# Performance work log

Measured on AMD Instinct MI355X. Metric: run time of the kernel, lower is better.

Reference implementation:

```python
import jax, jax.numpy as jnp
import numpy as np

B, N, NIN, NH, NOUT = 32, 64, 256, 256, 2
E = N * (N - 1)
BN_EPS = 1e-5


def _xavier(k, fan_in, fan_out):
    return jax.random.normal(k, (fan_in, fan_out), jnp.float32) * np.sqrt(2.0 / (fan_in + fan_out))


def _mlp_params(key, n_in, n_hid, n_out):
    k1, k2 = jax.random.split(key)
    return {
        'w1': _xavier(k1, n_in, n_hid), 'b1': jnp.full((n_hid,), 0.1, jnp.float32),
        'w2': _xavier(k2, n_hid, n_out), 'b2': jnp.full((n_out,), 0.1, jnp.float32),
        'g': jnp.ones((n_out,), jnp.float32), 'beta': jnp.zeros((n_out,), jnp.float32),
    }


def setup_inputs() -> dict:
    key = jax.random.key(0)
    ks = jax.random.split(key, 7)
    inputs = jax.random.normal(ks[0], (B, N, NIN), jnp.float32)
    # fully-connected directed graph w/o self loops: edge e = (send i, recv j), i != j
    idx = np.array([(i, j) for i in range(N) for j in range(N) if i != j], dtype=np.int64)
    rel_send = np.zeros((E, N), np.float32)
    rel_rec = np.zeros((E, N), np.float32)
    rel_send[np.arange(E), idx[:, 0]] = 1.0
    rel_rec[np.arange(E), idx[:, 1]] = 1.0
    out = {'inputs': inputs, 'rel_rec': jnp.asarray(rel_rec), 'rel_send': jnp.asarray(rel_send)}
    for name, (ni, nh, no), k in [('mlp1', (NIN, NH, NH), ks[1]),
                                  ('mlp2', (2 * NH, NH, NH), ks[2]),
                                  ('mlp3', (NH, NH, NH), ks[3]),
                                  ('mlp4', (3 * NH, NH, NH), ks[4])]:
        p = _mlp_params(k, ni, nh, no)
        for pk, pv in p.items():
            out[f'{name}_{pk}'] = pv
    out['fc_w'] = _xavier(ks[5], NH, NOUT)
    out['fc_b'] = jnp.full((NOUT,), 0.1, jnp.float32)
    return out


def _mlp(x, w1, b1, w2, b2, g, beta):
    # Linear -> ELU -> Linear -> ELU -> BatchNorm1d (training-mode batch stats, biased var)
    h = jax.nn.elu(x @ w1 + b1)
    h = jax.nn.elu(h @ w2 + b2)
    mean = h.mean(axis=(0, 1))
    var = h.var(axis=(0, 1))
    return (h - mean) * jax.lax.rsqrt(var + BN_EPS) * g + beta


def reference(inputs, rel_rec, rel_send,
              mlp1_w1, mlp1_b1, mlp1_w2, mlp1_b2, mlp1_g, mlp1_beta,
              mlp2_w1, mlp2_b1, mlp2_w2, mlp2_b2, mlp2_g, mlp2_beta,
              mlp3_w1, mlp3_b1, mlp3_w2, mlp3_b2, mlp3_g, mlp3_beta,
              mlp4_w1, mlp4_b1, mlp4_w2, mlp4_b2, mlp4_g, mlp4_beta,
              fc_w, fc_b):
    x = _mlp(inputs, mlp1_w1, mlp1_b1, mlp1_w2, mlp1_b2, mlp1_g, mlp1_beta)  # [B,N,NH]
    # node2edge: gather sender/receiver node features per edge
    s = jnp.einsum('en,bnh->beh', rel_send, x)
    r = jnp.einsum('en,bnh->beh', rel_rec, x)
    x = jnp.concatenate([s, r], axis=-1)  # [B,E,2*NH]
    x = _mlp(x, mlp2_w1, mlp2_b1, mlp2_w2, mlp2_b2, mlp2_g, mlp2_beta)
    x_skip = x
    # edge2node: scatter-sum incoming edges per node, normalized by N
    inc = jnp.einsum('en,beh->bnh', rel_rec, x) / N
    x = _mlp(inc, mlp3_w1, mlp3_b1, mlp3_w2, mlp3_b2, mlp3_g, mlp3_beta)
    s = jnp.einsum('en,bnh->beh', rel_send, x)
    r = jnp.einsum('en,bnh->beh', rel_rec, x)
    x = jnp.concatenate([s, r, x_skip], axis=-1)  # [B,E,3*NH]
    x = _mlp(x, mlp4_w1, mlp4_b1, mlp4_w2, mlp4_b2, mlp4_g, mlp4_beta)
    return x @ fc_w + fc_b  # [B,E,NOUT]
```

## Files before the change

kernel.cpp:

```cpp
#include <hip/hip_runtime.h>

typedef __bf16 bf16_t;
typedef __bf16 bf16x8 __attribute__((ext_vector_type(8)));
typedef float  f32x4  __attribute__((ext_vector_type(4)));

#define NB    64
#define EB    4032
#define BATCH 32
#define H     256
#define M_EDGE (BATCH*EB)
#define M_NODE (BATCH*NB)
#define T2    4
#define BN_EPS 1e-5f

__device__ __forceinline__ void load_lds16(const void* g, void* l) {
    __builtin_amdgcn_global_load_lds(
        (const __attribute__((address_space(1))) unsigned int*)g,
        (__attribute__((address_space(3))) unsigned int*)l, 16, 0, 0);
}
__device__ __forceinline__ float elu(float v) { return v > 0.f ? v : __expf(v) - 1.f; }

template<bool AF32>
__global__ __launch_bounds__(256)
void fused_mlp(const void* __restrict__ A0v,
               const bf16_t* __restrict__ W1t, const float* __restrict__ b1,
               const bf16_t* __restrict__ W2t, const float* __restrict__ b2,
               bf16_t* __restrict__ out, float* __restrict__ stats)
{
    const int m0 = blockIdx.x * 64;
    const int tid = threadIdx.x, wave = tid >> 6, lane = tid & 63;
    const int l15 = lane & 15, quad = lane >> 4;
    const int row = tid >> 2;
    const int cx8 = (((tid & 3) ^ ((tid >> 3) & 3))) * 8;
    const int sl8 = (tid & 3) * 8;
    const int xq8 = (quad ^ ((l15 >> 1) & 3)) * 8;

    __shared__ bf16_t h1s[64 * 264];
    __shared__ bf16_t Bs[256 * 32];
    __shared__ float  sred[512];

    const bf16_t* A0 = (const bf16_t*)A0v;

    f32x4 acc1[4][4];
#pragma unroll
    for (int t = 0; t < 4; ++t)
#pragma unroll
        for (int u = 0; u < 4; ++u) acc1[t][u] = (f32x4){0.f, 0.f, 0.f, 0.f};

    for (int k0 = 0; k0 < 256; k0 += 32) {
        bf16_t* ldsA = h1s + wave * 512;
        if (AF32) {
            const float* af = (const float*)A0v + (size_t)(m0 + row) * 256 + k0 + cx8;
            float4 lo = *(const float4*)af;
            float4 hi = *(const float4*)(af + 4);
            bf16x8 v;
            v[0]=(bf16_t)lo.x; v[1]=(bf16_t)lo.y; v[2]=(bf16_t)lo.z; v[3]=(bf16_t)lo.w;
            v[4]=(bf16_t)hi.x; v[5]=(bf16_t)hi.y; v[6]=(bf16_t)hi.z; v[7]=(bf16_t)hi.w;
            *(bf16x8*)&h1s[row * 32 + sl8] = v;
        } else {
            load_lds16(A0 + (size_t)(m0 + row) * 256 + k0 + cx8, ldsA);
        }
#pragma unroll
        for (int p = 0; p < 4; ++p)
            load_lds16(W1t + (size_t)(p * 64 + row) * 256 + k0 + cx8,
                       Bs + (p * 256 + wave * 64) * 8);
        __syncthreads();
        bf16x8 afr[4], bfr[4];
#pragma unroll
        for (int t = 0; t < 4; ++t)
            afr[t] = *(const bf16x8*)&h1s[(t * 16 + l15) * 32 + xq8];
#pragma unroll
        for (int u = 0; u < 4; ++u)
            bfr[u] = *(const bf16x8*)&Bs[(wave * 64 + u * 16 + l15) * 32 + xq8];
#pragma unroll
        for (int t = 0; t < 4; ++t)
#pragma unroll
            for (int u = 0; u < 4; ++u)
                acc1[t][u] = __builtin_amdgcn_mfma_f32_16x16x32_bf16(afr[t], bfr[u], acc1[t][u], 0, 0, 0);
        __syncthreads();
    }

#pragma unroll
    for (int u = 0; u < 4; ++u) {
        int   col = wave * 64 + u * 16 + l15;
        float bv  = b1[col];
#pragma unroll
        for (int t = 0; t < 4; ++t)
#pragma unroll
            for (int r = 0; r < 4; ++r)
                h1s[(t * 16 + quad * 4 + r) * 264 + col] = (bf16_t)elu(acc1[t][u][r] + bv);
    }
    sred[tid] = 0.f; sred[256 + tid] = 0.f;
    __syncthreads();

    f32x4 acc2[4][4];
#pragma unroll
    for (int t = 0; t < 4; ++t)
#pragma unroll
        for (int u = 0; u < 4; ++u) acc2[t][u] = (f32x4){0.f, 0.f, 0.f, 0.f};

    for (int k0 = 0; k0 < 256; k0 += 32) {
#pragma unroll
        for (int p = 0; p < 4; ++p)
            load_lds16(W2t + (size_t)(p * 64 + row) * 256 + k0 + cx8,
                       Bs + (p * 256 + wave * 64) * 8);
        __syncthreads();
        bf16x8 afr[4], bfr[4];
#pragma unroll
        for (int t = 0; t < 4; ++t)
            afr[t] = *(const bf16x8*)&h1s[(t * 16 + l15) * 264 + k0 + quad * 8];
#pragma unroll
        for (int u = 0; u < 4; ++u)
            bfr[u] = *(const bf16x8*)&Bs[(wave * 64 + u * 16 + l15) * 32 + xq8];
#pragma unroll
        for (int t = 0; t < 4; ++t)
#pragma unroll
            for (int u = 0; u < 4; ++u)
                acc2[t][u] = __builtin_amdgcn_mfma_f32_16x16x32_bf16(afr[t], bfr[u], acc2[t][u], 0, 0, 0);
        __syncthreads();
    }

#pragma unroll
    for (int u = 0; u < 4; ++u) {
        int   col = wave * 64 + u * 16 + l15;
        float bv  = b2[col];
        float s = 0.f, q = 0.f;
#pragma unroll
        for (int t = 0; t < 4; ++t)
#pragma unroll
            for (int r = 0; r < 4; ++r) {
                float v = elu(acc2[t][u][r] + bv);
                h1s[(t * 16 + quad * 4 + r) * 264 + col] = (bf16_t)v;
                s += v; q += v * v;
            }
        s += __shfl_xor(s, 16); s += __shfl_xor(s, 32);
        q += __shfl_xor(q, 16); q += __shfl_xor(q, 32);
        if (quad == 0) { atomicAdd(&sred[col], s); atomicAdd(&sred[256 + col], q); }
    }
    __syncthreads();
#pragma unroll
    for (int p = 0; p < 8; ++p) {
        int idx = p * 256 + tid;
        int r = idx >> 5, ch = idx & 31;
        *(uint4*)&out[(size_t)(m0 + r) * H + ch * 8] = *(const uint4*)&h1s[r * 264 + ch * 8];
    }
    atomicAdd(&stats[tid],     sred[tid]);
    atomicAdd(&stats[H + tid], sred[256 + tid]);
}

__global__ __launch_bounds__(256)
void node_gemm(const bf16_t* __restrict__ A, const float* __restrict__ statsIn,
               const float* __restrict__ g, const float* __restrict__ beta, float Mcnt,
               const bf16_t* __restrict__ Wt, const float* __restrict__ bias,
               float* __restrict__ out)
{
    const int m0 = blockIdx.x * 64;
    const int nb = blockIdx.y * 256;
    const int tid = threadIdx.x, wave = tid >> 6, lane = tid & 63;
    const int l15 = lane & 15, quad = lane >> 4;
    const int row = tid >> 2;
    const int cx8 = (((tid & 3) ^ ((tid >> 3) & 3))) * 8;
    const int sl8 = (tid & 3) * 8;
    const int xq8 = (quad ^ ((l15 >> 1) & 3)) * 8;
    __shared__ bf16_t As[64 * 32];
    __shared__ bf16_t Bs[256 * 32];
    __shared__ float  ss[512];

    {
        float mean = statsIn[tid] / Mcnt;
        float var  = statsIn[256 + tid] / Mcnt - mean * mean;
        float scl  = g[tid] * rsqrtf(var + BN_EPS);
        ss[tid]       = scl;
        ss[256 + tid] = beta[tid] - mean * scl;
    }
    __syncthreads();

    f32x4 acc[4][4];
#pragma unroll
    for (int t = 0; t < 4; ++t)
#pragma unroll
        for (int u = 0; u < 4; ++u) acc[t][u] = (f32x4){0.f, 0.f, 0.f, 0.f};

    for (int k0 = 0; k0 < 256; k0 += 32) {
        {
            int kc = k0 + cx8;
            bf16x8 v = *(const bf16x8*)(A + (size_t)(m0 + row) * 256 + kc);
            bf16x8 w;
#pragma unroll
            for (int j = 0; j < 8; ++j)
                w[j] = (bf16_t)((float)v[j] * ss[kc + j] + ss[256 + kc + j]);
            *(bf16x8*)&As[row * 32 + sl8] = w;
        }
#pragma unroll
        for (int p = 0; p < 4; ++p)
            load_lds16(Wt + (size_t)(nb + p * 64 + row) * 256 + k0 + cx8,
                       Bs + (p * 256 + wave * 64) * 8);
        __syncthreads();
        bf16x8 afr[4], bfr[4];
#pragma unroll
        for (int t = 0; t < 4; ++t)
            afr[t] = *(const bf16x8*)&As[(t * 16 + l15) * 32 + xq8];
#pragma unroll
        for (int u = 0; u < 4; ++u)
            bfr[u] = *(const bf16x8*)&Bs[(wave * 64 + u * 16 + l15) * 32 + xq8];
#pragma unroll
        for (int t = 0; t < 4; ++t)
#pragma unroll
            for (int u = 0; u < 4; ++u)
                acc[t][u] = __builtin_amdgcn_mfma_f32_16x16x32_bf16(afr[t], bfr[u], acc[t][u], 0, 0, 0);
        __syncthreads();
    }
#pragma unroll
    for (int u = 0; u < 4; ++u) {
        int col = nb + wave * 64 + u * 16 + l15;
        float bv = bias[col];
#pragma unroll
        for (int t = 0; t < 4; ++t)
#pragma unroll
            for (int r = 0; r < 4; ++r)
                out[(size_t)(m0 + t * 16 + quad * 4 + r) * 512 + col] = acc[t][u][r] + bv;
    }
}

__global__ __launch_bounds__(256, 2)
void m2_kernel(const float* __restrict__ PQ, const bf16_t* __restrict__ W2t,
               const float* __restrict__ b2, bf16_t* __restrict__ out,
               float* __restrict__ stats)
{
    const int tile0 = blockIdx.x * T2;
    const int tid = threadIdx.x, wave = tid >> 6, lane = tid & 63;
    const int l15 = lane & 15, quad = lane >> 4;

    __shared__ bf16_t Abuf[2][64 * 264];
    __shared__ float  sred[512];

    bf16x8 Breg[32];
#pragma unroll
    for (int ks = 0; ks < 8; ++ks)
#pragma unroll
        for (int u = 0; u < 4; ++u) {
            int col = wave * 64 + u * 16 + l15;
            Breg[ks * 4 + u] = *(const bf16x8*)(W2t + (size_t)col * 256 + ks * 32 + quad * 8);
        }
    sred[tid] = 0.f; sred[256 + tid] = 0.f;

    auto computeA = [&](int t, int b) {
        int row = tid >> 2;
        int m = (tile0 + t) * 64 + row;
        int bb = m / EB, e = m - bb * EB;
        int sn = e / (NB - 1), rr = e - sn * (NB - 1);
        int rc = rr + (rr >= sn ? 1 : 0);
        const float* Prow = PQ + (size_t)(bb * NB + sn) * 512;
        const float* Qrow = PQ + (size_t)(bb * NB + rc) * 512 + 256;
        int c0 = (tid & 3) * 64;
#pragma unroll
        for (int j = 0; j < 8; ++j) {
            int c = c0 + j * 8;
            float4 p0 = *(const float4*)(Prow + c);
            float4 p1 = *(const float4*)(Prow + c + 4);
            float4 q0 = *(const float4*)(Qrow + c);
            float4 q1 = *(const float4*)(Qrow + c + 4);
            bf16x8 v;
            v[0]=(bf16_t)elu(p0.x+q0.x); v[1]=(bf16_t)elu(p0.y+q0.y);
            v[2]=(bf16_t)elu(p0.z+q0.z); v[3]=(bf16_t)elu(p0.w+q0.w);
            v[4]=(bf16_t)elu(p1.x+q1.x); v[5]=(bf16_t)elu(p1.y+q1.y);
            v[6]=(bf16_t)elu(p1.z+q1.z); v[7]=(bf16_t)elu(p1.w+q1.w);
            *(bf16x8*)&Abuf[b][row * 264 + c] = v;
        }
    };

    computeA(0, 0);
    __syncthreads();

    for (int t = 0; t < T2; ++t) {
        const int cur = t & 1, nxt = cur ^ 1;
        if (t + 1 < T2) computeA(t + 1, nxt);

        f32x4 acc[4][4];
#pragma unroll
        for (int a = 0; a < 4; ++a)
#pragma unroll
            for (int u = 0; u < 4; ++u) acc[a][u] = (f32x4){0.f, 0.f, 0.f, 0.f};
#pragma unroll
        for (int ks = 0; ks < 8; ++ks) {
            bf16x8 afr[4];
#pragma unroll
            for (int a = 0; a < 4; ++a)
                afr[a] = *(const bf16x8*)&Abuf[cur][(a * 16 + l15) * 264 + ks * 32 + quad * 8];
#pragma unroll
            for (int a = 0; a < 4; ++a)
#pragma unroll
                for (int u = 0; u < 4; ++u)
                    acc[a][u] = __builtin_amdgcn_mfma_f32_16x16x32_bf16(afr[a], Breg[ks * 4 + u], acc[a][u], 0, 0, 0);
        }
        __syncthreads();

#pragma unroll
        for (int u = 0; u < 4; ++u) {
            int   col = wave * 64 + u * 16 + l15;
            float bv  = b2[col];
            float s = 0.f, q = 0.f;
#pragma unroll
            for (int a = 0; a < 4; ++a)
#pragma unroll
                for (int r = 0; r < 4; ++r) {
                    float v = elu(acc[a][u][r] + bv);
                    Abuf[cur][(a * 16 + quad * 4 + r) * 264 + col] = (bf16_t)v;
                    s += v; q += v * v;
                }
            s += __shfl_xor(s, 16); s += __shfl_xor(s, 32);
            q += __shfl_xor(q, 16); q += __shfl_xor(q, 32);
            if (quad == 0) { atomicAdd(&sred[col], s); atomicAdd(&sred[256 + col], q); }
        }
        __syncthreads();

        size_t m0 = (size_t)(tile0 + t) * 64;
#pragma unroll
        for (int p = 0; p < 8; ++p) {
            int idx = p * 256 + tid;
            int r = idx >> 5, ch = idx & 31;
            *(uint4*)&out[(m0 + r) * H + ch * 8] = *(const uint4*)&Abuf[cur][r * 264 + ch * 8];
        }
        __syncthreads();
    }
    atomicAdd(&stats[tid],     sred[tid]);
    atomicAdd(&stats[H + tid], sred[256 + tid]);
}

__global__ __launch_bounds__(256, 2)
void m4_kernel(const bf16_t* __restrict__ h2, const bf16_t* __restrict__ Wskt,
               const float* __restrict__ RS, const bf16_t* __restrict__ W2t,
               const float* __restrict__ b2, bf16_t* __restrict__ out,
               float* __restrict__ stats)
{
    const int m0 = blockIdx.x * 64;
    const int tid = threadIdx.x, wave = tid >> 6, lane = tid & 63;
    const int l15 = lane & 15, quad = lane >> 4;
    const int row = tid >> 2;
    const int c0 = (tid & 3) * 64;

    __shared__ bf16_t h1s[64 * 264];
    __shared__ float  sred[512];

    bf16x8 Breg[32];
#pragma unroll
    for (int ks = 0; ks < 8; ++ks)
#pragma unroll
        for (int u = 0; u < 4; ++u) {
            int col = wave * 64 + u * 16 + l15;
            Breg[ks * 4 + u] = *(const bf16x8*)(Wskt + (size_t)col * 256 + ks * 32 + quad * 8);
        }
    sred[tid] = 0.f; sred[256 + tid] = 0.f;

    {
        const bf16_t* src = h2 + (size_t)(m0 + row) * 256;
#pragma unroll
        for (int j = 0; j < 8; ++j) {
            int c = c0 + j * 8;
            *(bf16x8*)&h1s[row * 264 + c] = *(const bf16x8*)(src + c);
        }
    }
    __syncthreads();

    f32x4 acc[4][4];
#pragma unroll
    for (int a = 0; a < 4; ++a)
#pragma unroll
        for (int u = 0; u < 4; ++u) acc[a][u] = (f32x4){0.f, 0.f, 0.f, 0.f};

#pragma unroll
    for (int ks = 0; ks < 8; ++ks) {
        bf16x8 afr[4];
#pragma unroll
        for (int a = 0; a < 4; ++a)
            afr[a] = *(const bf16x8*)&h1s[(a * 16 + l15) * 264 + ks * 32 + quad * 8];
#pragma unroll
        for (int a = 0; a < 4; ++a)
#pragma unroll
            for (int u = 0; u < 4; ++u)
                acc[a][u] = __builtin_amdgcn_mfma_f32_16x16x32_bf16(afr[a], Breg[ks * 4 + u], acc[a][u], 0, 0, 0);
    }

#pragma unroll
    for (int ks = 0; ks < 8; ++ks)
#pragma unroll
        for (int u = 0; u < 4; ++u) {
            int col = wave * 64 + u * 16 + l15;
            Breg[ks * 4 + u] = *(const bf16x8*)(W2t + (size_t)col * 256 + ks * 32 + quad * 8);
        }
    __syncthreads();

#pragma unroll
    for (int u = 0; u < 4; ++u) {
        int col = wave * 64 + u * 16 + l15;
#pragma unroll
        for (int a = 0; a < 4; ++a)
#pragma unroll
            for (int r = 0; r < 4; ++r)
                h1s[(a * 16 + quad * 4 + r) * 264 + col] = (bf16_t)acc[a][u][r];
    }
    __syncthreads();

    {
        int m = m0 + row;
        int bb = m / EB, e = m - bb * EB;
        int sn = e / (NB - 1), rr = e - sn * (NB - 1);
        int rc = rr + (rr >= sn ? 1 : 0);
        const float* Srow = RS + (size_t)(bb * NB + sn) * 512;
        const float* Rrow = RS + (size_t)(bb * NB + rc) * 512 + 256;
#pragma unroll
        for (int j = 0; j < 8; ++j) {
            int c = c0 + j * 8;
            bf16x8 h = *(const bf16x8*)&h1s[row * 264 + c];
            float4 s0 = *(const float4*)(Srow + c);
            float4 s1 = *(const float4*)(Srow + c + 4);
            float4 r0 = *(const float4*)(Rrow + c);
            float4 r1 = *(const float4*)(Rrow + c + 4);
            bf16x8 v;
            v[0]=(bf16_t)elu((float)h[0]+s0.x+r0.x); v[1]=(bf16_t)elu((float)h[1]+s0.y+r0.y);
            v[2]=(bf16_t)elu((float)h[2]+s0.z+r0.z); v[3]=(bf16_t)elu((float)h[3]+s0.w+r0.w);
            v[4]=(bf16_t)elu((float)h[4]+s1.x+r1.x); v[5]=(bf16_t)elu((float)h[5]+s1.y+r1.y);
            v[6]=(bf16_t)elu((float)h[6]+s1.z+r1.z); v[7]=(bf16_t)elu((float)h[7]+s1.w+r1.w);
            *(bf16x8*)&h1s[row * 264 + c] = v;
        }
    }
    __syncthreads();

#pragma unroll
    for (int a = 0; a < 4; ++a)
#pragma unroll
        for (int u = 0; u < 4; ++u) acc[a][u] = (f32x4){0.f, 0.f, 0.f, 0.f};
#pragma unroll
    for (int ks = 0; ks < 8; ++ks) {
        bf16x8 afr[4];
#pragma unroll
        for (int a = 0; a < 4; ++a)
            afr[a] = *(const bf16x8*)&h1s[(a * 16 + l15) * 264 + ks * 32 + quad * 8];
#pragma unroll
        for (int a = 0; a < 4; ++a)
#pragma unroll
            for (int u = 0; u < 4; ++u)
                acc[a][u] = __builtin_amdgcn_mfma_f32_16x16x32_bf16(afr[a], Breg[ks * 4 + u], acc[a][u], 0, 0, 0);
    }
    __syncthreads();

#pragma unroll
    for (int u = 0; u < 4; ++u) {
        int   col = wave * 64 + u * 16 + l15;
        float bv  = b2[col];
        float s = 0.f, q = 0.f;
#pragma unroll
        for (int a = 0; a < 4; ++a)
#pragma unroll
            for (int r = 0; r < 4; ++r) {
                float v = elu(acc[a][u][r] + bv);
                h1s[(a * 16 + quad * 4 + r) * 264 + col] = (bf16_t)v;
                s += v; q += v * v;
            }
        s += __shfl_xor(s, 16); s += __shfl_xor(s, 32);
        q += __shfl_xor(q, 16); q += __shfl_xor(q, 32);
        if (quad == 0) { atomicAdd(&sred[col], s); atomicAdd(&sred[256 + col], q); }
    }
    __syncthreads();

#pragma unroll
    for (int p = 0; p < 8; ++p) {
        int idx = p * 256 + tid;
        int r = idx >> 5, ch = idx & 31;
        *(uint4*)&out[(size_t)(m0 + r) * H + ch * 8] = *(const uint4*)&h1s[r * 264 + ch * 8];
    }
    atomicAdd(&stats[tid],     sred[tid]);
    atomicAdd(&stats[H + tid], sred[256 + tid]);
}

__global__ void prep(const float* __restrict__ w1a, bf16_t* __restrict__ wt1a,
                     const float* __restrict__ w1b, bf16_t* __restrict__ wt1b,
                     const float* __restrict__ w2b, bf16_t* __restrict__ wt2b,
                     const float* __restrict__ w3a, bf16_t* __restrict__ wt3a,
                     const float* __restrict__ w3b, bf16_t* __restrict__ wt3b,
                     const float* __restrict__ w4b, bf16_t* __restrict__ wt4b,
                     const float* __restrict__ w2a, bf16_t* __restrict__ wtpq,
                     const float* __restrict__ w4a, bf16_t* __restrict__ wtrs,
                     const float* __restrict__ b2a, float* __restrict__ biasPQ,
                     float* __restrict__ stats)
{
    int blk = blockIdx.x, tid = threadIdx.x;
    if (blk < 1536) {
        int grp = blk >> 8, lb = blk & 255;
        const float* w; bf16_t* wt;
        switch (grp) {
            case 0: w = w1a; wt = wt1a; break;
            case 1: w = w1b; wt = wt1b; break;
            case 2: w = w2b; wt = wt2b; break;
            case 3: w = w3a; wt = wt3a; break;
            case 4: w = w3b; wt = wt3b; break;
            default: w = w4b; wt = wt4b; break;
        }
        int idx = lb * 256 + tid;
        int k = idx >> 8, n = idx & 255;
        wt[n * 256 + k] = (bf16_t)w[idx];
    } else if (blk < 2560) {
        int lb = blk - 1536;
        const float* w = (lb < 512) ? w2a : w4a;
        bf16_t* wt = (lb < 512) ? wtpq : wtrs;
        int c = lb & 511, k = tid;
        float v = (c < 256) ? w[k * 256 + c] : w[(256 + k) * 256 + (c - 256)];
        wt[c * 256 + k] = (bf16_t)v;
    } else if (blk == 2560) {
        biasPQ[tid] = b2a[tid];
        biasPQ[256 + tid] = 0.f;
    } else {
        for (int j = 0; j < 8; ++j) stats[j * 256 + tid] = 0.f;
    }
}

__global__ void prep2(const float* __restrict__ w4a, const float* __restrict__ stats2,
                      const float* __restrict__ g2, const float* __restrict__ be2,
                      const float* __restrict__ b4a, bf16_t* __restrict__ wt,
                      float* __restrict__ bias)
{
    __shared__ float sh2s[256];
    int blk = blockIdx.x, tid = threadIdx.x;
    float mean = stats2[tid] / (float)M_EDGE;
    float var  = stats2[256 + tid] / (float)M_EDGE - mean * mean;
    float scl  = g2[tid] * rsqrtf(var + BN_EPS);
    if (blk < 256) {
        wt[blk * 256 + tid] = (bf16_t)(w4a[(512 + tid) * 256 + blk] * scl);
    } else {
        sh2s[tid] = be2[tid] - mean * scl;
        __syncthreads();
        float acc = 0.f;
        for (int k = 0; k < 256; ++k)
            acc += sh2s[k] * w4a[(512 + k) * 256 + tid];
        bias[tid] = b4a[tid] + acc;
        bias[256 + tid] = 0.f;
    }
}

__global__ void edge2node(const bf16_t* __restrict__ x2, const float* __restrict__ stats2,
                          const float* __restrict__ g2, const float* __restrict__ be2,
                          bf16_t* __restrict__ inc)
{
    int bn = blockIdx.x, bb = bn >> 6, n = bn & 63;
    int g = threadIdx.x >> 5, t = threadIdx.x & 31;
    __shared__ float part[8][256];
    __shared__ float ss[512];
    {
        int c = threadIdx.x;
        float mean = stats2[c] / (float)M_EDGE;
        float var  = stats2[256 + c] / (float)M_EDGE - mean * mean;
        float scl  = g2[c] * rsqrtf(var + BN_EPS);
        ss[c]       = scl;
        ss[256 + c] = be2[c] - mean * scl;
    }
    const bf16_t* base = x2 + (size_t)bb * EB * H;
    float a[8] = {0.f,0.f,0.f,0.f,0.f,0.f,0.f,0.f};
    for (int i = g; i < NB; i += 8) {
        if (i == n) continue;
        int e = i * (NB - 1) + n - (n > i ? 1 : 0);
        bf16x8 v = *(const bf16x8*)&base[(size_t)e * H + t * 8];
#pragma unroll
        for (int j = 0; j < 8; ++j) a[j] += (float)v[j];
    }
#pragma unroll
    for (int j = 0; j < 8; ++j) part[g][t * 8 + j] = a[j];
    __syncthreads();
    int c = threadIdx.x;
    float s = 0.f;
#pragma unroll
    for (int g2i = 0; g2i < 8; ++g2i) s += part[g2i][c];
    inc[(size_t)bn * H + c] = (bf16_t)(s * (1.f / 64.f) * ss[c] + ss[256 + c] * (63.f / 64.f));
}

__global__ void fc_kernel(const bf16_t* __restrict__ x4, const float* __restrict__ stats4,
                          const float* __restrict__ g4, const float* __restrict__ be4,
                          const float* __restrict__ fcw, const float* __restrict__ fcb,
                          float* __restrict__ out)
{
    __shared__ float ss[512];
    {
        int c = threadIdx.x;
        float mean = stats4[c] / (float)M_EDGE;
        float var  = stats4[256 + c] / (float)M_EDGE - mean * mean;
        float scl  = g4[c] * rsqrtf(var + BN_EPS);
        ss[c]       = scl;
        ss[256 + c] = be4[c] - mean * scl;
    }
    __syncthreads();
    int row  = blockIdx.x * 8 + (threadIdx.x >> 5);
    int t    = threadIdx.x & 31;
    bf16x8 v8 = *(const bf16x8*)(x4 + (size_t)row * H + t * 8);
    float s0 = 0.f, s1 = 0.f;
#pragma unroll
    for (int j = 0; j < 8; ++j) {
        int c = t * 8 + j;
        float v = (float)v8[j] * ss[c] + ss[256 + c];
        s0 += v * fcw[c * 2];
        s1 += v * fcw[c * 2 + 1];
    }
#pragma unroll
    for (int off = 16; off; off >>= 1) {
        s0 += __shfl_down(s0, off, 32);
        s1 += __shfl_down(s1, off, 32);
    }
    if (t == 0) {
        out[(size_t)row * 2]     = s0 + fcb[0];
        out[(size_t)row * 2 + 1] = s1 + fcb[1];
    }
}

extern "C" void kernel_launch(void* const* d_in, const int* in_sizes, int n_in,
                              void* d_out, int out_size, void* d_ws, size_t ws_size,
                              hipStream_t stream)
{
    (void)in_sizes; (void)n_in; (void)out_size; (void)ws_size;
    const float* inp = (const float*)d_in[0];
    const float* w1a = (const float*)d_in[3];  const float* b1a = (const float*)d_in[4];
    const float* w1b = (const float*)d_in[5];  const float* b1b = (const float*)d_in[6];
    const float* g1  = (const float*)d_in[7];  const float* be1 = (const float*)d_in[8];
    const float* w2a = (const float*)d_in[9];  const float* b2a = (const float*)d_in[10];
    const float* w2b = (const float*)d_in[11]; const float* b2b = (const float*)d_in[12];
    const float* g2  = (const float*)d_in[13]; const float* be2 = (const float*)d_in[14];
    const float* w3a = (const float*)d_in[15]; const float* b3a = (const float*)d_in[16];
    const float* w3b = (const float*)d_in[17]; const float* b3b = (const float*)d_in[18];
    const float* g3  = (const float*)d_in[19]; const float* be3 = (const float*)d_in[20];
    const float* w4a = (const float*)d_in[21]; const float* b4a = (const float*)d_in[22];
    const float* w4b = (const float*)d_in[23]; const float* b4b = (const float*)d_in[24];
    const float* g4  = (const float*)d_in[25]; const float* be4 = (const float*)d_in[26];
    const float* fcw = (const float*)d_in[27]; const float* fcb = (const float*)d_in[28];

    char* p = (char*)d_ws;
    auto alloc = [&](size_t nbytes) { char* r = p; p += (nbytes + 255) & ~(size_t)255; return r; };

    bf16_t* wt1a = (bf16_t*)alloc(256 * 256 * 2);
    bf16_t* wt1b = (bf16_t*)alloc(256 * 256 * 2);
    bf16_t* wt2b = (bf16_t*)alloc(256 * 256 * 2);
    bf16_t* wt3a = (bf16_t*)alloc(256 * 256 * 2);
    bf16_t* wt3b = (bf16_t*)alloc(256 * 256 * 2);
    bf16_t* wt4b = (bf16_t*)alloc(256 * 256 * 2);
    bf16_t* wtpq = (bf16_t*)alloc(512 * 256 * 2);
    bf16_t* wtrs = (bf16_t*)alloc(512 * 256 * 2);
    bf16_t* wtsk = (bf16_t*)alloc(256 * 256 * 2);
    float*  biasPQ = (float*)alloc(512 * sizeof(float));
    float*  biasRS = (float*)alloc(512 * sizeof(float));
    float*  stats  = (float*)alloc(4 * 512 * sizeof(float));
    bf16_t* x1   = (bf16_t*)alloc((size_t)M_NODE * H * 2);
    bf16_t* incb = (bf16_t*)alloc((size_t)M_NODE * H * 2);
    bf16_t* x3   = (bf16_t*)alloc((size_t)M_NODE * H * 2);
    float*  PQ   = (float*)alloc((size_t)M_NODE * 512 * sizeof(float));
    float*  RS   = (float*)alloc((size_t)M_NODE * 512 * sizeof(float));
    bf16_t* h2   = (bf16_t*)alloc((size_t)M_EDGE * H * 2);
    bf16_t* h4   = (bf16_t*)alloc((size_t)M_EDGE * H * 2);

    prep<<<2562, 256, 0, stream>>>(w1a, wt1a, w1b, wt1b, w2b, wt2b, w3a, wt3a,
                                   w3b, wt3b, w4b, wt4b, w2a, wtpq, w4a, wtrs,
                                   b2a, biasPQ, stats);

    fused_mlp<true ><<<M_NODE / 64, 256, 0, stream>>>(inp, wt1a, b1a, wt1b, b1b, x1, stats + 0);

    { dim3 g(M_NODE / 64, 2);
      node_gemm<<<g, 256, 0, stream>>>(x1, stats + 0, g1, be1, (float)M_NODE, wtpq, biasPQ, PQ); }

    m2_kernel<<<M_EDGE / (64 * T2), 256, 0, stream>>>(PQ, wt2b, b2b, h2, stats + 512);

    edge2node<<<M_NODE, 256, 0, stream>>>(h2, stats + 512, g2, be2, incb);
    fused_mlp<false><<<M_NODE / 64, 256, 0, stream>>>(incb, wt3a, b3a, wt3b, b3b, x3, stats + 1024);

    prep2<<<257, 256, 0, stream>>>(w4a, stats + 512, g2, be2, b4a, wtsk, biasRS);
    { dim3 g(M_NODE / 64, 2);
      node_gemm<<<g, 256, 0, stream>>>(x3, stats + 1024, g3, be3, (float)M_NODE, wtrs, biasRS, RS); }

    m4_kernel<<<M_EDGE / 64, 256, 0, stream>>>(h2, wtsk, RS, wt4b, b4b, h4, stats + 1536);

    fc_kernel<<<M_EDGE / 8, 256, 0, stream>>>(h4, stats + 1536, g4, be4, fcw, fcb, (float*)d_out);
}
```

Before: 394.6 us.

## Make m4_kernel persistent over four tiles, streaming W2 through double-buffered LDS

m4_kernel now processes T4=4 row tiles per block. The skip-weight fragment is loaded into registers once and reused across all tiles, and per-block stats atomics are amortized. The second GEMM's weights are no longer held in registers. They are streamed per k-slice into a double-buffered, XOR-swizzled LDS buffer with global_load_lds, which lowers register pressure. The trade-off is more LDS traffic, extra barriers per k-step, and a quarter as many blocks, which reduces parallelism.

```diff
diff --git a/kernel.cpp b/kernel.cpp
--- a/kernel.cpp
+++ b/kernel.cpp
@@ -11,6 +11,7 @@
 #define M_EDGE (BATCH*EB)
 #define M_NODE (BATCH*NB)
 #define T2    4
+#define T4    4
 #define BN_EPS 1e-5f
 
 __device__ __forceinline__ void load_lds16(const void* g, void* l) {
@@ -333,13 +334,16 @@
                const float* __restrict__ b2, bf16_t* __restrict__ out,
                float* __restrict__ stats)
 {
-    const int m0 = blockIdx.x * 64;
+    const int tile0 = blockIdx.x * T4;
     const int tid = threadIdx.x, wave = tid >> 6, lane = tid & 63;
     const int l15 = lane & 15, quad = lane >> 4;
     const int row = tid >> 2;
     const int c0 = (tid & 3) * 64;
+    const int cx8 = (((tid & 3) ^ ((tid >> 3) & 3))) * 8;
+    const int xq8 = (quad ^ ((l15 >> 1) & 3)) * 8;
 
     __shared__ bf16_t h1s[64 * 264];
+    __shared__ bf16_t Bs[2][256 * 32];
     __shared__ float  sred[512];
 
     bf16x8 Breg[32];
@@ -351,123 +355,136 @@
             Breg[ks * 4 + u] = *(const bf16x8*)(Wskt + (size_t)col * 256 + ks * 32 + quad * 8);
         }
     sred[tid] = 0.f; sred[256 + tid] = 0.f;
-
-    {
-        const bf16_t* src = h2 + (size_t)(m0 + row) * 256;
-#pragma unroll
-        for (int j = 0; j < 8; ++j) {
-            int c = c0 + j * 8;
-            *(bf16x8*)&h1s[row * 264 + c] = *(const bf16x8*)(src + c);
-        }
-    }
     __syncthreads();
 
-    f32x4 acc[4][4];
-#pragma unroll
-    for (int a = 0; a < 4; ++a)
-#pragma unroll
-        for (int u = 0; u < 4; ++u) acc[a][u] = (f32x4){0.f, 0.f, 0.f, 0.f};
-
-#pragma unroll
-    for (int ks = 0; ks < 8; ++ks) {
-        bf16x8 afr[4];
+    for (int t = 0; t < T4; ++t) {
+        const int m0 = (tile0 + t) * 64;
+
+        {
+            const bf16_t* src = h2 + (size_t)(m0 + row) * 256;
+#pragma unroll
+            for (int j = 0; j < 8; ++j) {
+                int c = c0 + j * 8;
+                *(bf16x8*)&h1s[row * 264 + c] = *(const bf16x8*)(src + c);
+            }
+        }
+        __syncthreads();
+
+        f32x4 acc[4][4];
 #pragma unroll
         for (int a = 0; a < 4; ++a)
-            afr[a] = *(const bf16x8*)&h1s[(a * 16 + l15) * 264 + ks * 32 + quad * 8];
-#pragma unroll
-        for (int a = 0; a < 4; ++a)
-#pragma unroll
-            for (int u = 0; u < 4; ++u)
-                acc[a][u] = __builtin_amdgcn_mfma_f32_16x16x32_bf16(afr[a], Breg[ks * 4 + u], acc[a][u], 0, 0, 0);
-    }
-
-#pragma unroll
-    for (int ks = 0; ks < 8; ++ks)
+#pragma unroll
+            for (int u = 0; u < 4; ++u) acc[a][u] = (f32x4){0.f, 0.f, 0.f, 0.f};
+
+#pragma unroll
+        for (int ks = 0; ks < 8; ++ks) {
+            bf16x8 afr[4];
+#pragma unroll
+            for (int a = 0; a < 4; ++a)
+                afr[a] = *(const bf16x8*)&h1s[(a * 16 + l15) * 264 + ks * 32 + quad * 8];
+#pragma unroll
+            for (int a = 0; a < 4; ++a)
+#pragma unroll
+                for (int u = 0; u < 4; ++u)
+                    acc[a][u] = __builtin_amdgcn_mfma_f32_16x16x32_bf16(afr[a], Breg[ks * 4 + u], acc[a][u], 0, 0, 0);
+        }
+
+#pragma unroll
+        for (int p = 0; p < 4; ++p)
+            load_lds16(W2t + (size_t)(p * 64 + row) * 256 + 0 + cx8,
+                       Bs[0] + (p * 256 + wave * 64) * 8);
+        __syncthreads();
+
 #pragma unroll
         for (int u = 0; u < 4; ++u) {
             int col = wave * 64 + u * 16 + l15;
-            Breg[ks * 4 + u] = *(const bf16x8*)(W2t + (size_t)col * 256 + ks * 32 + quad * 8);
-        }
-    __syncthreads();
-
-#pragma unroll
-    for (int u = 0; u < 4; ++u) {
-        int col = wave * 64 + u * 16 + l15;
+#pragma unroll
+            for (int a = 0; a < 4; ++a)
+#pragma unroll
+                for (int r = 0; r < 4; ++r)
+                    h1s[(a * 16 + quad * 4 + r) * 264 + col] = (bf16_t)acc[a][u][r];
+        }
+        __syncthreads();
+
+        {
+            int m = m0 + row;
+            int bb = m / EB, e = m - bb * EB;
+            int sn = e / (NB - 1), rr = e - sn * (NB - 1);
+            int rc = rr + (rr >= sn ? 1 : 0);
+            const float* Srow = RS + (size_t)(bb * NB + sn) * 512;
+            const float* Rrow = RS + (size_t)(bb * NB + rc) * 512 + 256;
+#pragma unroll
+            for (int j = 0; j < 8; ++j) {
+                int c = c0 + j * 8;
+                bf16x8 h = *(const bf16x8*)&h1s[row * 264 + c];
+                float4 s0 = *(const float4*)(Srow + c);
+                float4 s1 = *(const float4*)(Srow + c + 4);
+                float4 r0 = *(const float4*)(Rrow + c);
+                float4 r1 = *(const float4*)(Rrow + c + 4);
+                bf16x8 v;
+                v[0]=(bf16_t)elu((float)h[0]+s0.x+r0.x); v[1]=(bf16_t)elu((float)h[1]+s0.y+r0.y);
+                v[2]=(bf16_t)elu((float)h[2]+s0.z+r0.z); v[3]=(bf16_t)elu((float)h[3]+s0.w+r0.w);
+                v[4]=(bf16_t)elu((float)h[4]+s1.x+r1.x); v[5]=(bf16_t)elu((float)h[5]+s1.y+r1.y);
+                v[6]=(bf16_t)elu((float)h[6]+s1.z+r1.z); v[7]=(bf16_t)elu((float)h[7]+s1.w+r1.w);
+                *(bf16x8*)&h1s[row * 264 + c] = v;
+            }
+        }
+        __syncthreads();
+
 #pragma unroll
         for (int a = 0; a < 4; ++a)
 #pragma unroll
-            for (int r = 0; r < 4; ++r)
-                h1s[(a * 16 + quad * 4 + r) * 264 + col] = (bf16_t)acc[a][u][r];
-    }
-    __syncthreads();
-
-    {
-        int m = m0 + row;
-        int bb = m / EB, e = m - bb * EB;
-        int sn = e / (NB - 1), rr = e - sn * (NB - 1);
-        int rc = rr + (rr >= sn ? 1 : 0);
-        const float* Srow = RS + (size_t)(bb * NB + sn) * 512;
-        const float* Rrow = RS + (size_t)(bb * NB + rc) * 512 + 256;
-#pragma unroll
-        for (int j = 0; j < 8; ++j) {
-            int c = c0 + j * 8;
-            bf16x8 h = *(const bf16x8*)&h1s[row * 264 + c];
-            float4 s0 = *(const float4*)(Srow + c);
-            float4 s1 = *(const float4*)(Srow + c + 4);
-            float4 r0 = *(const float4*)(Rrow + c);
-            float4 r1 = *(const float4*)(Rrow + c + 4);
-            bf16x8 v;
-            v[0]=(bf16_t)elu((float)h[0]+s0.x+r0.x); v[1]=(bf16_t)elu((float)h[1]+s0.y+r0.y);
-            v[2]=(bf16_t)elu((float)h[2]+s0.z+r0.z); v[3]=(bf16_t)elu((float)h[3]+s0.w+r0.w);
-            v[4]=(bf16_t)elu((float)h[4]+s1.x+r1.x); v[5]=(bf16_t)elu((float)h[5]+s1.y+r1.y);
-            v[6]=(bf16_t)elu((float)h[6]+s1.z+r1.z); v[7]=(bf16_t)elu((float)h[7]+s1.w+r1.w);
-            *(bf16x8*)&h1s[row * 264 + c] = v;
-        }
-    }
-    __syncthreads();
-
-#pragma unroll
-    for (int a = 0; a < 4; ++a)
-#pragma unroll
-        for (int u = 0; u < 4; ++u) acc[a][u] = (f32x4){0.f, 0.f, 0.f, 0.f};
-#pragma unroll
-    for (int ks = 0; ks < 8; ++ks) {
-        bf16x8 afr[4];
-#pragma unroll
-        for (int a = 0; a < 4; ++a)
-            afr[a] = *(const bf16x8*)&h1s[(a * 16 + l15) * 264 + ks * 32 + quad * 8];
-#pragma unroll
-        for (int a = 0; a < 4; ++a)
+            for (int u = 0; u < 4; ++u) acc[a][u] = (f32x4){0.f, 0.f, 0.f, 0.f};
+#pragma unroll
+        for (int ks = 0; ks < 8; ++ks) {
+            const int cb = ks & 1;
+            if (ks + 1 < 8) {
+#pragma unroll
+                for (int p = 0; p < 4; ++p)
+                    load_lds16(W2t + (size_t)(p * 64 + row) * 256 + (ks + 1) * 32 + cx8,
+                               Bs[cb ^ 1] + (p * 256 + wave * 64) * 8);
+            }
+            bf16x8 afr[4], bfr[4];
+#pragma unroll
+            for (int a = 0; a < 4; ++a)
+                afr[a] = *(const bf16x8*)&h1s[(a * 16 + l15) * 264 + ks * 32 + quad * 8];
 #pragma unroll
             for (int u = 0; u < 4; ++u)
-                acc[a][u] = __builtin_amdgcn_mfma_f32_16x16x32_bf16(afr[a], Breg[ks * 4 + u], acc[a][u], 0, 0, 0);
-    }
-    __syncthreads();
-
-#pragma unroll
-    for (int u = 0; u < 4; ++u) {
-        int   col = wave * 64 + u * 16 + l15;
-        float bv  = b2[col];
-        float s = 0.f, q = 0.f;
-#pragma unroll
-        for (int a = 0; a < 4; ++a)
-#pragma unroll
-            for (int r = 0; r < 4; ++r) {
-                float v = elu(acc[a][u][r] + bv);
-                h1s[(a * 16 + quad * 4 + r) * 264 + col] = (bf16_t)v;
-                s += v; q += v * v;
-            }
-        s += __shfl_xor(s, 16); s += __shfl_xor(s, 32);
-        q += __shfl_xor(q, 16); q += __shfl_xor(q, 32);
-        if (quad == 0) { atomicAdd(&sred[col], s); atomicAdd(&sred[256 + col], q); }
-    }
-    __syncthreads();
-
-#pragma unroll
-    for (int p = 0; p < 8; ++p) {
-        int idx = p * 256 + tid;
-        int r = idx >> 5, ch = idx & 31;
-        *(uint4*)&out[(size_t)(m0 + r) * H + ch * 8] = *(const uint4*)&h1s[r * 264 + ch * 8];
+                bfr[u] = *(const bf16x8*)&Bs[cb][(wave * 64 + u * 16 + l15) * 32 + xq8];
+#pragma unroll
+            for (int a = 0; a < 4; ++a)
+#pragma unroll
+                for (int u = 0; u < 4; ++u)
+                    acc[a][u] = __builtin_amdgcn_mfma_f32_16x16x32_bf16(afr[a], bfr[u], acc[a][u], 0, 0, 0);
+            __syncthreads();
+        }
+
+#pragma unroll
+        for (int u = 0; u < 4; ++u) {
+            int   col = wave * 64 + u * 16 + l15;
+            float bv  = b2[col];
+            float s = 0.f, q = 0.f;
+#pragma unroll
+            for (int a = 0; a < 4; ++a)
+#pragma unroll
+                for (int r = 0; r < 4; ++r) {
+                    float v = elu(acc[a][u][r] + bv);
+                    h1s[(a * 16 + quad * 4 + r) * 264 + col] = (bf16_t)v;
+                    s += v; q += v * v;
+                }
+            s += __shfl_xor(s, 16); s += __shfl_xor(s, 32);
+            q += __shfl_xor(q, 16); q += __shfl_xor(q, 32);
+            if (quad == 0) { atomicAdd(&sred[col], s); atomicAdd(&sred[256 + col], q); }
+        }
+        __syncthreads();
+
+#pragma unroll
+        for (int p = 0; p < 8; ++p) {
+            int idx = p * 256 + tid;
+            int r = idx >> 5, ch = idx & 31;
+            *(uint4*)&out[(size_t)(m0 + r) * H + ch * 8] = *(const uint4*)&h1s[r * 264 + ch * 8];
+        }
+        __syncthreads();
     }
     atomicAdd(&stats[tid],     sred[tid]);
     atomicAdd(&stats[H + tid], sred[256 + tid]);
@@ -670,7 +687,7 @@
     { dim3 g(M_NODE / 64, 2);
       node_gemm<<<g, 256, 0, stream>>>(x3, stats + 1024, g3, be3, (float)M_NODE, wtrs, biasRS, RS); }
 
-    m4_kernel<<<M_EDGE / 64, 256, 0, stream>>>(h2, wtsk, RS, wt4b, b4b, h4, stats + 1536);
+    m4_kernel<<<M_EDGE / (64 * T4), 256, 0, stream>>>(h2, wtsk, RS, wt4b, b4b, h4, stats + 1536);
 
     fc_kernel<<<M_EDGE / 8, 256, 0, stream>>>(h4, stats + 1536, g4, be4, fcw, fcb, (float*)d_out);
 }
```

After: 419.8 us. 6.4% more time.

## Stream fragment-packed weights per k-step in m4_kernel to raise occupancy

Applied to the files above, without the earlier changes.

m4_kernel used to hold all 32 B-fragments (the whole per-wave weight slice) in registers. It now streams four fragments per k-step with double-buffered prefetch, and the launch bound rises from 2 to 3 blocks per CU. The prep and prep2 kernels now write the skip weight and the mlp4 second-layer weight in a wave/ks/u/lane fragment layout, so each lane's load is contiguous and coalesced. This trades a single register-resident weight set for repeated global/L2 weight loads inside the MFMA loop, in exchange for lower VGPR pressure and more resident waves.

```diff
diff --git a/kernel.cpp b/kernel.cpp
--- a/kernel.cpp
+++ b/kernel.cpp
@@ -327,9 +327,9 @@
     atomicAdd(&stats[H + tid], sred[256 + tid]);
 }
 
-__global__ __launch_bounds__(256, 2)
-void m4_kernel(const bf16_t* __restrict__ h2, const bf16_t* __restrict__ Wskt,
-               const float* __restrict__ RS, const bf16_t* __restrict__ W2t,
+__global__ __launch_bounds__(256, 3)
+void m4_kernel(const bf16_t* __restrict__ h2, const bf16_t* __restrict__ Wskf,
+               const float* __restrict__ RS, const bf16_t* __restrict__ W4f,
                const float* __restrict__ b2, bf16_t* __restrict__ out,
                float* __restrict__ stats)
 {
@@ -342,14 +342,6 @@
     __shared__ bf16_t h1s[64 * 264];
     __shared__ float  sred[512];
 
-    bf16x8 Breg[32];
-#pragma unroll
-    for (int ks = 0; ks < 8; ++ks)
-#pragma unroll
-        for (int u = 0; u < 4; ++u) {
-            int col = wave * 64 + u * 16 + l15;
-            Breg[ks * 4 + u] = *(const bf16x8*)(Wskt + (size_t)col * 256 + ks * 32 + quad * 8);
-        }
     sred[tid] = 0.f; sred[256 + tid] = 0.f;
 
     {
@@ -360,6 +352,14 @@
             *(bf16x8*)&h1s[row * 264 + c] = *(const bf16x8*)(src + c);
         }
     }
+
+    const bf16_t* WskW = Wskf + (size_t)wave * 16384;
+    const bf16_t* W4W  = W4f  + (size_t)wave * 16384;
+
+    bf16x8 bcur[4], bnxt[4];
+#pragma unroll
+    for (int u = 0; u < 4; ++u)
+        bcur[u] = *(const bf16x8*)(WskW + u * 512 + lane * 8);
     __syncthreads();
 
     f32x4 acc[4][4];
@@ -370,6 +370,11 @@
 
 #pragma unroll
     for (int ks = 0; ks < 8; ++ks) {
+        if (ks < 7) {
+#pragma unroll
+            for (int u = 0; u < 4; ++u)
+                bnxt[u] = *(const bf16x8*)(WskW + (ks + 1) * 2048 + u * 512 + lane * 8);
+        }
         bf16x8 afr[4];
 #pragma unroll
         for (int a = 0; a < 4; ++a)
@@ -378,16 +383,14 @@
         for (int a = 0; a < 4; ++a)
 #pragma unroll
             for (int u = 0; u < 4; ++u)
-                acc[a][u] = __builtin_amdgcn_mfma_f32_16x16x32_bf16(afr[a], Breg[ks * 4 + u], acc[a][u], 0, 0, 0);
-    }
-
-#pragma unroll
-    for (int ks = 0; ks < 8; ++ks)
-#pragma unroll
-        for (int u = 0; u < 4; ++u) {
-            int col = wave * 64 + u * 16 + l15;
-            Breg[ks * 4 + u] = *(const bf16x8*)(W2t + (size_t)col * 256 + ks * 32 + quad * 8);
-        }
+                acc[a][u] = __builtin_amdgcn_mfma_f32_16x16x32_bf16(afr[a], bcur[u], acc[a][u], 0, 0, 0);
+#pragma unroll
+        for (int u = 0; u < 4; ++u) bcur[u] = bnxt[u];
+    }
+
+#pragma unroll
+    for (int u = 0; u < 4; ++u)
+        bcur[u] = *(const bf16x8*)(W4W + u * 512 + lane * 8);
     __syncthreads();
 
 #pragma unroll
@@ -432,6 +435,11 @@
         for (int u = 0; u < 4; ++u) acc[a][u] = (f32x4){0.f, 0.f, 0.f, 0.f};
 #pragma unroll
     for (int ks = 0; ks < 8; ++ks) {
+        if (ks < 7) {
+#pragma unroll
+            for (int u = 0; u < 4; ++u)
+                bnxt[u] = *(const bf16x8*)(W4W + (ks + 1) * 2048 + u * 512 + lane * 8);
+        }
         bf16x8 afr[4];
 #pragma unroll
         for (int a = 0; a < 4; ++a)
@@ -440,7 +448,9 @@
         for (int a = 0; a < 4; ++a)
 #pragma unroll
             for (int u = 0; u < 4; ++u)
-                acc[a][u] = __builtin_amdgcn_mfma_f32_16x16x32_bf16(afr[a], Breg[ks * 4 + u], acc[a][u], 0, 0, 0);
+                acc[a][u] = __builtin_amdgcn_mfma_f32_16x16x32_bf16(afr[a], bcur[u], acc[a][u], 0, 0, 0);
+#pragma unroll
+        for (int u = 0; u < 4; ++u) bcur[u] = bnxt[u];
     }
     __syncthreads();
 
@@ -487,18 +497,23 @@
     int blk = blockIdx.x, tid = threadIdx.x;
     if (blk < 1536) {
         int grp = blk >> 8, lb = blk & 255;
-        const float* w; bf16_t* wt;
-        switch (grp) {
-            case 0: w = w1a; wt = wt1a; break;
-            case 1: w = w1b; wt = wt1b; break;
-            case 2: w = w2b; wt = wt2b; break;
-            case 3: w = w3a; wt = wt3a; break;
-            case 4: w = w3b; wt = wt3b; break;
-            default: w = w4b; wt = wt4b; break;
-        }
         int idx = lb * 256 + tid;
         int k = idx >> 8, n = idx & 255;
-        wt[n * 256 + k] = (bf16_t)w[idx];
+        if (grp == 5) {
+            int wv = n >> 6, u = (n >> 4) & 3, l15 = n & 15;
+            int ks = k >> 5, qd = (k >> 3) & 3, j = k & 7;
+            wt4b[wv * 16384 + ks * 2048 + u * 512 + (qd * 16 + l15) * 8 + j] = (bf16_t)w4b[idx];
+        } else {
+            const float* w; bf16_t* wt;
+            switch (grp) {
+                case 0: w = w1a; wt = wt1a; break;
+                case 1: w = w1b; wt = wt1b; break;
+                case 2: w = w2b; wt = wt2b; break;
+                case 3: w = w3a; wt = wt3a; break;
+                default: w = w3b; wt = wt3b; break;
+            }
+            wt[n * 256 + k] = (bf16_t)w[idx];
+        }
     } else if (blk < 2560) {
         int lb = blk - 1536;
         const float* w = (lb < 512) ? w2a : w4a;
@@ -525,7 +540,11 @@
     float var  = stats2[256 + tid] / (float)M_EDGE - mean * mean;
     float scl  = g2[tid] * rsqrtf(var + BN_EPS);
     if (blk < 256) {
-        wt[blk * 256 + tid] = (bf16_t)(w4a[(512 + tid) * 256 + blk] * scl);
+        int n = blk, k = tid;
+        int wv = n >> 6, u = (n >> 4) & 3, l15 = n & 15;
+        int ks = k >> 5, qd = (k >> 3) & 3, j = k & 7;
+        wt[wv * 16384 + ks * 2048 + u * 512 + (qd * 16 + l15) * 8 + j] =
+            (bf16_t)(w4a[(512 + tid) * 256 + blk] * scl);
     } else {
         sh2s[tid] = be2[tid] - mean * scl;
         __syncthreads();
```

Result: faster. 372.1 us (-5.7%).
